# Kernel optimization log

Hardware: AMD Instinct MI355X
Metric: run time of the kernel (lower is better)

## Reference

```python
import jax, jax.numpy as jnp
import numpy as np

IOU_THRESHOLD = 0.5
NEG_POS_RATIO = 3
CENTER_VARIANCE = 0.1
SIZE_VARIANCE = 0.2


def _corner_to_center(b):
    return jnp.concatenate([(b[..., :2] + b[..., 2:]) * 0.5, b[..., 2:] - b[..., :2]], axis=-1)


def _area(lt, rb):
    wh = jnp.clip(rb - lt, 0.0)
    return wh[..., 0] * wh[..., 1]


def _iou(boxes0, boxes1, eps=1e-5):
    lt = jnp.maximum(boxes0[..., :2], boxes1[..., :2])
    rb = jnp.minimum(boxes0[..., 2:], boxes1[..., 2:])
    inter = _area(lt, rb)
    a0 = _area(boxes0[..., :2], boxes0[..., 2:])
    a1 = _area(boxes1[..., :2], boxes1[..., 2:])
    return inter / (a0 + a1 - inter + eps)


def _match_one(gt_boxes, gt_labels, valid, anchors_corner, anchors_center):
    # gt_boxes [G,4] corner, gt_labels [G], valid [G] bool, anchors [A,4]
    G = gt_boxes.shape[0]
    A = anchors_corner.shape[0]
    ious = _iou(gt_boxes[:, None, :], anchors_corner[None, :, :])  # [G, A]
    ious = jnp.where(valid[:, None], ious, -1.0)  # mask padded gts
    best_target_iou = ious.max(axis=0)            # [A]
    best_target_idx = ious.argmax(axis=0)         # [A]
    best_prior_idx = ious.argmax(axis=1)          # [G]
    # force-assign each valid gt to its best anchor (invalid rows -> OOB, dropped)
    safe_prior = jnp.where(valid, best_prior_idx, A)
    best_target_idx = best_target_idx.at[safe_prior].set(jnp.arange(G), mode='drop')
    best_target_iou = best_target_iou.at[safe_prior].set(2.0, mode='drop')
    labels = jnp.where(best_target_iou < IOU_THRESHOLD, 0, gt_labels[best_target_idx])
    boxes_c = _corner_to_center(gt_boxes[best_target_idx])  # [A,4] center form
    loc = jnp.concatenate([
        (boxes_c[:, :2] - anchors_center[:, :2]) / anchors_center[:, 2:] / CENTER_VARIANCE,
        jnp.log(jnp.clip(boxes_c[:, 2:] / anchors_center[:, 2:], 1e-8)) / SIZE_VARIANCE,
    ], axis=-1)
    return labels, loc


def _multibox_loss(confidence, predicted_locations, gts, counts, anchors):
    B, A, C = confidence.shape
    G = gts.shape[1]
    gt_boxes = gts[..., :4]
    gt_labels = gts[..., 4].astype(jnp.int32)
    valid = jnp.arange(G)[None, :] < counts[:, None]  # [B, G]
    anchors_center = _corner_to_center(anchors)
    labels, gt_locations = jax.vmap(_match_one, in_axes=(0, 0, 0, None, None))(
        gt_boxes, gt_labels, valid, anchors, anchors_center)  # [B,A], [B,A,4]

    log_probs = jax.nn.log_softmax(confidence, axis=2)  # [B, A, C]
    bg_loss = -log_probs[:, :, 0]                       # [B, A]
    pos_mask = labels > 0
    num_pos_row = pos_mask.sum(axis=1, keepdims=True)   # [B, 1]
    # hard negative mining: rank background losses per row, keep top 3*num_pos
    mining = jnp.where(pos_mask, -jnp.inf, bg_loss)
    order = jnp.argsort(-mining, axis=1)
    rank = jnp.argsort(order, axis=1)
    neg_mask = rank < num_pos_row * NEG_POS_RATIO
    mask = pos_mask | neg_mask

    num_pos = jnp.maximum(1.0, pos_mask.sum().astype(confidence.dtype))
    ce = -jnp.take_along_axis(log_probs, labels[..., None], axis=2)[..., 0]  # [B, A]
    classification_loss = jnp.where(mask, ce, 0.0).sum() / (num_pos * 4.0)

    diff = jnp.abs(predicted_locations - gt_locations)
    smooth_l1 = jnp.where(diff < 1.0, 0.5 * diff * diff, diff - 0.5)
    localisation_loss = (smooth_l1 * pos_mask[..., None]).sum() / (num_pos * 4.0)
    return localisation_loss, classification_loss


def setup_inputs() -> dict:
    key = jax.random.key(0)
    ks = jax.random.split(key, 8)
    B, A, G, C = 32, 32768, 50, 22
    confidence = jax.random.normal(ks[0], (B, A, C), jnp.float32)
    predicted_locations = jax.random.normal(ks[1], (B, A, 4), jnp.float32)
    a_c = jax.random.uniform(ks[2], (A, 2), minval=0.05, maxval=0.95)
    a_wh = jax.random.uniform(ks[3], (A, 2), minval=0.02, maxval=0.3)
    anchors = jnp.concatenate([jnp.clip(a_c - a_wh * 0.5, 0.0, 1.0),
                               jnp.clip(a_c + a_wh * 0.5, 0.0, 1.0)], axis=-1)
    g_c = jax.random.uniform(ks[4], (B, G, 2), minval=0.1, maxval=0.9)
    g_wh = jax.random.uniform(ks[5], (B, G, 2), minval=0.05, maxval=0.4)
    g_boxes = jnp.concatenate([jnp.clip(g_c - g_wh * 0.5, 0.0, 1.0),
                               jnp.clip(g_c + g_wh * 0.5, 0.0, 1.0)], axis=-1)
    g_labels = jax.random.randint(ks[6], (B, G), 1, C).astype(jnp.float32)
    gts = jnp.concatenate([g_boxes, g_labels[..., None]], axis=-1)
    counts = jax.random.randint(ks[7], (B,), 1, G + 1).astype(jnp.int32)
    return {"confidence": confidence, "predicted_locations": predicted_locations,
            "gts": gts, "counts": counts, "anchors": anchors}


def reference(confidence, predicted_locations, gts, counts, anchors):
    return _multibox_loss(confidence, predicted_locations, gts, counts, anchors)
```

## Files before the change

kernel.cpp:

```cpp
#include <hip/hip_runtime.h>
#include <cstdint>
#include <cstddef>

#define B_N 32
#define A_N 32768
#define G_N 50
#define C_N 22
#define BA  (B_N * A_N)

#define GC 4
#define NCHUNK ((G_N + GC - 1) / GC)
#define ASEG 16
#define ASEG_LEN (A_N / ASEG)

#define SEL_CAP 4096


__device__ __forceinline__ float iou_one(float gx0, float gy0, float gx1, float gy1, float ga,
                                         float ax0, float ay0, float ax1, float ay1, float aa) {
    float lx = fmaxf(gx0, ax0), ly = fmaxf(gy0, ay0);
    float rx = fminf(gx1, ax1), ry = fminf(gy1, ay1);
    float iw = fmaxf(rx - lx, 0.0f), ih = fmaxf(ry - ly, 0.0f);
    float inter = iw * ih;
    return inter / (ga + aa - inter + 1e-5f);
}

__device__ __forceinline__ unsigned int f2key(float x) {
    unsigned int u = __float_as_uint(x);
    return (u & 0x80000000u) ? ~u : (u | 0x80000000u);
}

__device__ __forceinline__ float key2f(unsigned int k) {
    return __uint_as_float((k & 0x80000000u) ? (k & 0x7FFFFFFFu) : ~k);
}


__global__ void init_kernel(float* hdr, unsigned long long* bp_best) {
    if (threadIdx.x < 128) hdr[threadIdx.x] = 0.0f;
    for (int i = threadIdx.x; i < B_N * G_N; i += 256) bp_best[i] = 0ull;
}

__global__ __launch_bounds__(256) void best_prior_kernel(
        const float* __restrict__ gts, const int* __restrict__ counts,
        const float* __restrict__ anchors, unsigned long long* __restrict__ bp_best) {
    int blk = blockIdx.x;
    int b   = blk / (NCHUNK * ASEG);
    int rem = blk % (NCHUNK * ASEG);
    int ch  = rem / ASEG;
    int seg = rem % ASEG;
    int g0  = ch * GC;
    int cnt = counts[b];
    if (g0 >= cnt) return;
    float gx0[GC], gy0[GC], gx1[GC], gy1[GC], ga[GC];
    #pragma unroll
    for (int j = 0; j < GC; ++j) {
        if (g0 + j < cnt) {
            const float* p = gts + (size_t)(b * G_N + g0 + j) * 5;
            gx0[j] = p[0]; gy0[j] = p[1]; gx1[j] = p[2]; gy1[j] = p[3];
            ga[j] = fmaxf(gx1[j] - gx0[j], 0.0f) * fmaxf(gy1[j] - gy0[j], 0.0f);
        } else { gx0[j] = 0.f; gy0[j] = 0.f; gx1[j] = 0.f; gy1[j] = 0.f; ga[j] = 0.f; }
    }
    unsigned long long best[GC];
    #pragma unroll
    for (int j = 0; j < GC; ++j) best[j] = 0ull;
    int a0 = seg * ASEG_LEN;
    for (int a = a0 + threadIdx.x; a < a0 + ASEG_LEN; a += 256) {
        float4 an = reinterpret_cast<const float4*>(anchors)[a];
        float aa = fmaxf(an.z - an.x, 0.0f) * fmaxf(an.w - an.y, 0.0f);
        #pragma unroll
        for (int j = 0; j < GC; ++j) {
            float iou = iou_one(gx0[j], gy0[j], gx1[j], gy1[j], ga[j],
                                an.x, an.y, an.z, an.w, aa);
            unsigned long long key = ((unsigned long long)f2key(iou) << 32) | (unsigned)(~a);
            if (key > best[j]) best[j] = key;
        }
    }
    #pragma unroll
    for (int j = 0; j < GC; ++j) {
        for (int o = 32; o > 0; o >>= 1) {
            unsigned long long other = __shfl_down(best[j], o, 64);
            if (other > best[j]) best[j] = other;
        }
    }
    if ((threadIdx.x & 63) == 0) {
        int ng = cnt - g0; if (ng > GC) ng = GC;
        for (int j = 0; j < ng; ++j)
            atomicMax(&bp_best[b * G_N + g0 + j], best[j]);
    }
}

__global__ __launch_bounds__(256) void fused_kernel(
        const float* __restrict__ gts, const int* __restrict__ counts,
        const float* __restrict__ anchors, const float* __restrict__ pred_loc,
        const float* __restrict__ conf, const unsigned long long* __restrict__ bp_best,
        float* __restrict__ mining, float* __restrict__ loc_part,
        float* __restrict__ ce_part, int* __restrict__ num_pos_row) {
    int blk = blockIdx.x;
    int tid = threadIdx.x;
    int i = blk * 256 + tid;
    int b = blk >> 7;
    int a = i & (A_N - 1);
    int cnt = counts[b];
    __shared__ float sc[256 * C_N];
    __shared__ float sg[G_N][5];
    __shared__ int   sl[G_N];
    __shared__ int   sp[G_N];

    {
        const float4* c4 = reinterpret_cast<const float4*>(conf) + (size_t)blk * (256 * C_N / 4);
        float4* s4 = reinterpret_cast<float4*>(sc);
        #pragma unroll
        for (int t = 0; t < 5; ++t) s4[tid + t * 256] = c4[tid + t * 256];
        if (tid < 128) s4[tid + 5 * 256] = c4[tid + 5 * 256];
    }
    if (tid < G_N) {
        int g = tid;
        const float* gtb = gts + (size_t)(b * G_N + g) * 5;
        float x0 = gtb[0], y0 = gtb[1], x1 = gtb[2], y1 = gtb[3];
        sg[g][0] = x0; sg[g][1] = y0; sg[g][2] = x1; sg[g][3] = y1;
        sg[g][4] = fmaxf(x1 - x0, 0.0f) * fmaxf(y1 - y0, 0.0f);
        sl[g] = (int)gtb[4];
        sp[g] = (int)(~(unsigned)(bp_best[b * G_N + g] & 0xFFFFFFFFull));
    }
    __syncthreads();

    float4 an = reinterpret_cast<const float4*>(anchors)[a];
    float aa = fmaxf(an.z - an.x, 0.0f) * fmaxf(an.w - an.y, 0.0f);
    float best = -2.0f; int gi = 0;
    for (int g = 0; g < cnt; ++g) {
        float iou = iou_one(sg[g][0], sg[g][1], sg[g][2], sg[g][3], sg[g][4],
                            an.x, an.y, an.z, an.w, aa);
        if (iou > best) { best = iou; gi = g; }
    }
    bool forced = false;
    for (int g = 0; g < cnt; ++g) {
        if (sp[g] == a) { gi = g; forced = true; }
    }
    float iou_eff = forced ? 2.0f : best;
    int label = 0;
    if (!(iou_eff < 0.5f)) label = sl[gi];
    bool pos = label > 0;

    float contrib = 0.0f;
    if (pos) {
        float acx = (an.x + an.z) * 0.5f, acy = (an.y + an.w) * 0.5f;
        float aw = an.z - an.x, ah = an.w - an.y;
        float gx0 = sg[gi][0], gy0 = sg[gi][1], gx1 = sg[gi][2], gy1 = sg[gi][3];
        float cx = (gx0 + gx1) * 0.5f, cy = (gy0 + gy1) * 0.5f;
        float w = gx1 - gx0, h = gy1 - gy0;
        float l0 = ((cx - acx) / aw) / 0.1f;
        float l1 = ((cy - acy) / ah) / 0.1f;
        float l2 = logf(fmaxf(w / aw, 1e-8f)) / 0.2f;
        float l3 = logf(fmaxf(h / ah, 1e-8f)) / 0.2f;
        float4 p = reinterpret_cast<const float4*>(pred_loc)[i];
        float d0 = fabsf(p.x - l0), d1 = fabsf(p.y - l1);
        float d2 = fabsf(p.z - l2), d3 = fabsf(p.w - l3);
        contrib  = (d0 < 1.0f ? 0.5f * d0 * d0 : d0 - 0.5f);
        contrib += (d1 < 1.0f ? 0.5f * d1 * d1 : d1 - 0.5f);
        contrib += (d2 < 1.0f ? 0.5f * d2 * d2 : d2 - 0.5f);
        contrib += (d3 < 1.0f ? 0.5f * d3 * d3 : d3 - 0.5f);
    }

    float v[C_N];
    {
        const float2* myrow = reinterpret_cast<const float2*>(sc + tid * C_N);
        #pragma unroll
        for (int j = 0; j < C_N / 2; ++j) { float2 t = myrow[j]; v[2 * j] = t.x; v[2 * j + 1] = t.y; }
    }
    float m = v[0];
    #pragma unroll
    for (int j = 1; j < C_N; ++j) m = fmaxf(m, v[j]);
    float s = 0.0f;
    #pragma unroll
    for (int j = 0; j < C_N; ++j) s += expf(v[j] - m);
    float ls = logf(s);
    float ce_pos = 0.0f;
    if (pos) {
        float vl = v[0];
        #pragma unroll
        for (int j = 1; j < C_N; ++j) vl = (j == label) ? v[j] : vl;
        ce_pos = ls - (vl - m);
        mining[i] = __int_as_float(0xFF800000);
    } else {
        mining[i] = ls - (v[0] - m);
    }

    unsigned long long bal = __ballot(pos);
    for (int o = 32; o > 0; o >>= 1) {
        contrib += __shfl_down(contrib, o, 64);
        ce_pos  += __shfl_down(ce_pos, o, 64);
    }
    __shared__ float swl[4], swc[4];
    __shared__ int   swi[4];
    int wid = tid >> 6, lane = tid & 63;
    if (lane == 0) { swl[wid] = contrib; swc[wid] = ce_pos; swi[wid] = __popcll(bal); }
    __syncthreads();
    if (tid == 0) {
        float sL = swl[0] + swl[1] + swl[2] + swl[3];
        float sC = swc[0] + swc[1] + swc[2] + swc[3];
        int   c  = swi[0] + swi[1] + swi[2] + swi[3];
        int slot = blk & 31;
        if (sL != 0.0f) atomicAdd(&loc_part[slot], sL);
        if (sC != 0.0f) atomicAdd(&ce_part[slot], sC);
        if (c) atomicAdd(&num_pos_row[b], c);
    }
}

__device__ __forceinline__ void scan_pick(unsigned* hist, int nwords,
                                          unsigned* sA, unsigned* sB,
                                          int krem, int* s_bin, int* s_krem) {
    int t = threadIdx.x;
    unsigned lo = 0, hi = 0;
    if (t < nwords) { unsigned w = hist[t]; lo = w & 0xFFFFu; hi = w >> 16; }
    sA[t] = lo + hi;
    __syncthreads();
    unsigned* src = sA; unsigned* dst = sB;
    for (int d = 1; d < 1024; d <<= 1) {
        unsigned vv = src[t] + ((t + d < 1024) ? src[t + d] : 0u);
        dst[t] = vv;
        __syncthreads();
        unsigned* tmp = src; src = dst; dst = tmp;
    }
    unsigned incl = src[t];
    unsigned incl_next = (t < 1023) ? src[t + 1] : 0u;
    unsigned uk = (unsigned)krem;
    if (incl >= uk && incl_next < uk) {
        unsigned cum = incl_next;
        if (cum + hi >= uk) { *s_bin = 2 * t + 1; *s_krem = (int)(uk - cum); }
        else                { *s_bin = 2 * t;     *s_krem = (int)(uk - cum - hi); }
    }
    __syncthreads();
}

__global__ __launch_bounds__(1024) void select_kernel(
        const float* __restrict__ mining, const int* __restrict__ num_pos_row,
        float* __restrict__ neg_sum) {
    int b = blockIdx.x;
    int tid = threadIdx.x;
    int np = num_pos_row[b];
    long long k = 3LL * np;
    int num_neg = A_N - np;
    int k_eff = (int)((k < (long long)num_neg) ? k : (long long)num_neg);
    if (k_eff <= 0) { if (tid == 0) neg_sum[b] = 0.0f; return; }
    const float4* row4 = reinterpret_cast<const float4*>(mining + (size_t)b * A_N);

    __shared__ unsigned hist[1024];
    __shared__ unsigned sA[1024], sB[1024];
    __shared__ unsigned surv[SEL_CAP];
    __shared__ int s_n1, s_bin, s_krem;
    __shared__ float swf[16];

    hist[tid] = 0;
    if (tid == 0) s_n1 = 0;
    __syncthreads();
    #pragma unroll
    for (int it = 0; it < A_N / 4 / 1024; ++it) {
        float4 vv = row4[tid + it * 1024];
        unsigned k0 = f2key(vv.x), k1 = f2key(vv.y), k2 = f2key(vv.z), k3 = f2key(vv.w);
        unsigned b0 = k0 >> 21, b1 = k1 >> 21, b2 = k2 >> 21, b3 = k3 >> 21;
        atomicAdd(&hist[b0 >> 1], (b0 & 1) ? 65536u : 1u);
        atomicAdd(&hist[b1 >> 1], (b1 & 1) ? 65536u : 1u);
        atomicAdd(&hist[b2 >> 1], (b2 & 1) ? 65536u : 1u);
        atomicAdd(&hist[b3 >> 1], (b3 & 1) ? 65536u : 1u);
    }
    __syncthreads();
    scan_pick(hist, 1024, sA, sB, k_eff, &s_bin, &s_krem);
    unsigned bin1 = (unsigned)s_bin;
    int krem1 = s_krem;
    __syncthreads();

    float sum_sel = 0.0f;
    #pragma unroll
    for (int it = 0; it < A_N / 4 / 1024; ++it) {
        float4 vv = row4[tid + it * 1024];
        float xs[4] = {vv.x, vv.y, vv.z, vv.w};
        #pragma unroll
        for (int e = 0; e < 4; ++e) {
            unsigned key = f2key(xs[e]);
            unsigned t11 = key >> 21;
            if (t11 > bin1) sum_sel += xs[e];
            else if (t11 == bin1) {
                int p = atomicAdd(&s_n1, 1);
                if (p < SEL_CAP) surv[p] = key;
            }
        }
    }
    __syncthreads();
    int n1 = s_n1;
    bool in_lds = (n1 <= SEL_CAP);

    hist[tid] = 0;
    __syncthreads();
    if (in_lds) {
        for (int ii = tid; ii < n1; ii += 1024) {
            unsigned bin = (surv[ii] >> 10) & 0x7FFu;
            atomicAdd(&hist[bin >> 1], (bin & 1) ? 65536u : 1u);
        }
    } else {
        for (int it = 0; it < A_N / 4 / 1024; ++it) {
            float4 vv = row4[tid + it * 1024];
            float xs[4] = {vv.x, vv.y, vv.z, vv.w};
            for (int e = 0; e < 4; ++e) {
                unsigned key = f2key(xs[e]);
                if ((key >> 21) == bin1) {
                    unsigned bin = (key >> 10) & 0x7FFu;
                    atomicAdd(&hist[bin >> 1], (bin & 1) ? 65536u : 1u);
                }
            }
        }
    }
    __syncthreads();
    scan_pick(hist, 1024, sA, sB, krem1, &s_bin, &s_krem);
    unsigned prefix22 = (bin1 << 11) | (unsigned)s_bin;
    int krem2 = s_krem;
    __syncthreads();

    hist[tid] = 0;
    __syncthreads();
    if (in_lds) {
        for (int ii = tid; ii < n1; ii += 1024) {
            unsigned key = surv[ii];
            if ((key >> 10) == prefix22) {
                unsigned bin = key & 0x3FFu;
                atomicAdd(&hist[bin >> 1], (bin & 1) ? 65536u : 1u);
            }
        }
    } else {
        for (int it = 0; it < A_N / 4 / 1024; ++it) {
            float4 vv = row4[tid + it * 1024];
            float xs[4] = {vv.x, vv.y, vv.z, vv.w};
            for (int e = 0; e < 4; ++e) {
                unsigned key = f2key(xs[e]);
                if ((key >> 10) == prefix22) {
                    unsigned bin = key & 0x3FFu;
                    atomicAdd(&hist[bin >> 1], (bin & 1) ? 65536u : 1u);
                }
            }
        }
    }
    __syncthreads();
    scan_pick(hist, 512, sA, sB, krem2, &s_bin, &s_krem);
    unsigned kth = (prefix22 << 10) | (unsigned)s_bin;
    int krem3 = s_krem;
    __syncthreads();

    if (in_lds) {
        for (int ii = tid; ii < n1; ii += 1024) {
            unsigned key = surv[ii];
            if (key > kth) sum_sel += key2f(key);
        }
    } else {
        for (int it = 0; it < A_N / 4 / 1024; ++it) {
            float4 vv = row4[tid + it * 1024];
            float xs[4] = {vv.x, vv.y, vv.z, vv.w};
            for (int e = 0; e < 4; ++e) {
                unsigned key = f2key(xs[e]);
                if ((key >> 21) == bin1 && key > kth) sum_sel += xs[e];
            }
        }
    }
    for (int o = 32; o > 0; o >>= 1) sum_sel += __shfl_down(sum_sel, o, 64);
    int wid = tid >> 6, lane = tid & 63;
    if (lane == 0) swf[wid] = sum_sel;
    __syncthreads();
    if (tid == 0) {
        float tot = 0.0f;
        #pragma unroll
        for (int w = 0; w < 16; ++w) tot += swf[w];
        neg_sum[b] = tot + (float)krem3 * key2f(kth);
    }
}

__global__ void final_kernel(const float* __restrict__ loc_part, const float* __restrict__ ce_part,
                             const int* __restrict__ num_pos_row, const float* __restrict__ neg_sum,
                             float* __restrict__ out) {
    if (threadIdx.x != 0) return;
    int tot = 0;
    for (int b = 0; b < B_N; ++b) tot += num_pos_row[b];
    float npos = fmaxf(1.0f, (float)tot);
    float L = 0.0f, Cp = 0.0f, Ng = 0.0f;
    for (int j = 0; j < B_N; ++j) { L += loc_part[j]; Cp += ce_part[j]; Ng += neg_sum[j]; }
    out[0] = L / (npos * 4.0f);
    out[1] = (Cp + Ng) / (npos * 4.0f);
}


extern "C" void kernel_launch(void* const* d_in, const int* in_sizes, int n_in,
                              void* d_out, int out_size, void* d_ws, size_t ws_size,
                              hipStream_t stream) {
    const float* conf     = (const float*)d_in[0];
    const float* pred_loc = (const float*)d_in[1];
    const float* gts      = (const float*)d_in[2];
    const int*   counts   = (const int*)d_in[3];
    const float* anchors  = (const float*)d_in[4];
    float* out = (float*)d_out;

    char* ws = (char*)d_ws;
    float* loc_part     = (float*)ws;
    float* ce_part      = (float*)(ws + 128);
    int*   num_pos_row  = (int*)(ws + 256);
    float* neg_sum      = (float*)(ws + 384);
    unsigned long long* bp_best = (unsigned long long*)(ws + 512);
    float* mining       = (float*)(ws + 16384);

    init_kernel<<<1, 256, 0, stream>>>(loc_part, bp_best);
    best_prior_kernel<<<B_N * NCHUNK * ASEG, 256, 0, stream>>>(gts, counts, anchors, bp_best);
    fused_kernel<<<BA / 256, 256, 0, stream>>>(gts, counts, anchors, pred_loc, conf, bp_best,
                                               mining, loc_part, ce_part, num_pos_row);
    select_kernel<<<B_N, 1024, 0, stream>>>(mining, num_pos_row, neg_sum);
    final_kernel<<<1, 64, 0, stream>>>(loc_part, ce_part, num_pos_row, neg_sum, out);
}
```

Baseline: 263.1 us.

## Process two anchors per thread, drop LDS conf staging, split fused launch

Each thread of the fused kernel now handles two anchors, so each shared gt box read serves two IoU evaluations. The shared-memory staging of confidence rows is removed and rows are read directly from global memory, which frees about 22 KB of LDS per block and may raise occupancy. The fused kernel is issued as four launches of 512 blocks using a block offset. The risks are uncoalesced strided conf loads, higher register pressure, and extra launch overhead.

```diff
diff --git a/kernel.cpp b/kernel.cpp
--- a/kernel.cpp
+++ b/kernel.cpp
@@ -89,30 +89,69 @@
     }
 }
 
+__device__ __forceinline__ void softmax_one(const float* __restrict__ conf, size_t i,
+                                            int lab, bool pos,
+                                            float* __restrict__ mining, float& ce_acc) {
+    float v[C_N];
+    const float2* c2 = reinterpret_cast<const float2*>(conf + i * C_N);
+    #pragma unroll
+    for (int j = 0; j < C_N / 2; ++j) { float2 t = c2[j]; v[2 * j] = t.x; v[2 * j + 1] = t.y; }
+    float m = v[0];
+    #pragma unroll
+    for (int j = 1; j < C_N; ++j) m = fmaxf(m, v[j]);
+    float s = 0.0f;
+    #pragma unroll
+    for (int j = 0; j < C_N; ++j) s += expf(v[j] - m);
+    float ls = logf(s);
+    if (pos) {
+        float vl = v[0];
+        #pragma unroll
+        for (int j = 1; j < C_N; ++j) vl = (j == lab) ? v[j] : vl;
+        ce_acc += ls - (vl - m);
+        mining[i] = __int_as_float(0xFF800000);
+    } else {
+        mining[i] = ls - (v[0] - m);
+    }
+}
+
+__device__ __forceinline__ float loc_term(float4 an, const float sgrow[5],
+                                          const float* __restrict__ pred_loc, size_t i) {
+    float acx = (an.x + an.z) * 0.5f, acy = (an.y + an.w) * 0.5f;
+    float aw = an.z - an.x, ah = an.w - an.y;
+    float gx0 = sgrow[0], gy0 = sgrow[1], gx1 = sgrow[2], gy1 = sgrow[3];
+    float cx = (gx0 + gx1) * 0.5f, cy = (gy0 + gy1) * 0.5f;
+    float w = gx1 - gx0, h = gy1 - gy0;
+    float l0 = ((cx - acx) / aw) / 0.1f;
+    float l1 = ((cy - acy) / ah) / 0.1f;
+    float l2 = logf(fmaxf(w / aw, 1e-8f)) / 0.2f;
+    float l3 = logf(fmaxf(h / ah, 1e-8f)) / 0.2f;
+    float4 p = reinterpret_cast<const float4*>(pred_loc)[i];
+    float d0 = fabsf(p.x - l0), d1 = fabsf(p.y - l1);
+    float d2 = fabsf(p.z - l2), d3 = fabsf(p.w - l3);
+    float c;
+    c  = (d0 < 1.0f ? 0.5f * d0 * d0 : d0 - 0.5f);
+    c += (d1 < 1.0f ? 0.5f * d1 * d1 : d1 - 0.5f);
+    c += (d2 < 1.0f ? 0.5f * d2 * d2 : d2 - 0.5f);
+    c += (d3 < 1.0f ? 0.5f * d3 * d3 : d3 - 0.5f);
+    return c;
+}
+
 __global__ __launch_bounds__(256) void fused_kernel(
         const float* __restrict__ gts, const int* __restrict__ counts,
         const float* __restrict__ anchors, const float* __restrict__ pred_loc,
         const float* __restrict__ conf, const unsigned long long* __restrict__ bp_best,
         float* __restrict__ mining, float* __restrict__ loc_part,
-        float* __restrict__ ce_part, int* __restrict__ num_pos_row) {
-    int blk = blockIdx.x;
+        float* __restrict__ ce_part, int* __restrict__ num_pos_row, int blk_off) {
+    int blk = blockIdx.x + blk_off;
     int tid = threadIdx.x;
-    int i = blk * 256 + tid;
-    int b = blk >> 7;
-    int a = i & (A_N - 1);
+    int b = blk >> 6;
+    int abase = (blk & 63) << 9;
+    int a0 = abase + tid, a1 = a0 + 256;
+    size_t i0 = (size_t)b * A_N + a0, i1 = i0 + 256;
     int cnt = counts[b];
-    __shared__ float sc[256 * C_N];
     __shared__ float sg[G_N][5];
     __shared__ int   sl[G_N];
     __shared__ int   sp[G_N];
-
-    {
-        const float4* c4 = reinterpret_cast<const float4*>(conf) + (size_t)blk * (256 * C_N / 4);
-        float4* s4 = reinterpret_cast<float4*>(sc);
-        #pragma unroll
-        for (int t = 0; t < 5; ++t) s4[tid + t * 256] = c4[tid + t * 256];
-        if (tid < 128) s4[tid + 5 * 256] = c4[tid + 5 * 256];
-    }
     if (tid < G_N) {
         int g = tid;
         const float* gtb = gts + (size_t)(b * G_N + g) * 5;
@@ -124,76 +163,49 @@
     }
     __syncthreads();
 
-    float4 an = reinterpret_cast<const float4*>(anchors)[a];
-    float aa = fmaxf(an.z - an.x, 0.0f) * fmaxf(an.w - an.y, 0.0f);
-    float best = -2.0f; int gi = 0;
+    float4 an0 = reinterpret_cast<const float4*>(anchors)[a0];
+    float4 an1 = reinterpret_cast<const float4*>(anchors)[a1];
+    float aa0 = fmaxf(an0.z - an0.x, 0.0f) * fmaxf(an0.w - an0.y, 0.0f);
+    float aa1 = fmaxf(an1.z - an1.x, 0.0f) * fmaxf(an1.w - an1.y, 0.0f);
+    float best0 = -2.0f, best1 = -2.0f;
+    int gi0 = 0, gi1 = 0;
     for (int g = 0; g < cnt; ++g) {
-        float iou = iou_one(sg[g][0], sg[g][1], sg[g][2], sg[g][3], sg[g][4],
-                            an.x, an.y, an.z, an.w, aa);
-        if (iou > best) { best = iou; gi = g; }
-    }
-    bool forced = false;
+        float x0 = sg[g][0], y0 = sg[g][1], x1 = sg[g][2], y1 = sg[g][3], ar = sg[g][4];
+        float iou0 = iou_one(x0, y0, x1, y1, ar, an0.x, an0.y, an0.z, an0.w, aa0);
+        float iou1 = iou_one(x0, y0, x1, y1, ar, an1.x, an1.y, an1.z, an1.w, aa1);
+        if (iou0 > best0) { best0 = iou0; gi0 = g; }
+        if (iou1 > best1) { best1 = iou1; gi1 = g; }
+    }
+    bool f0 = false, f1 = false;
     for (int g = 0; g < cnt; ++g) {
-        if (sp[g] == a) { gi = g; forced = true; }
-    }
-    float iou_eff = forced ? 2.0f : best;
-    int label = 0;
-    if (!(iou_eff < 0.5f)) label = sl[gi];
-    bool pos = label > 0;
+        int p = sp[g];
+        if (p == a0) { gi0 = g; f0 = true; }
+        if (p == a1) { gi1 = g; f1 = true; }
+    }
+    float ie0 = f0 ? 2.0f : best0;
+    float ie1 = f1 ? 2.0f : best1;
+    int lab0 = 0; if (!(ie0 < 0.5f)) lab0 = sl[gi0];
+    int lab1 = 0; if (!(ie1 < 0.5f)) lab1 = sl[gi1];
+    bool pos0 = lab0 > 0, pos1 = lab1 > 0;
 
     float contrib = 0.0f;
-    if (pos) {
-        float acx = (an.x + an.z) * 0.5f, acy = (an.y + an.w) * 0.5f;
-        float aw = an.z - an.x, ah = an.w - an.y;
-        float gx0 = sg[gi][0], gy0 = sg[gi][1], gx1 = sg[gi][2], gy1 = sg[gi][3];
-        float cx = (gx0 + gx1) * 0.5f, cy = (gy0 + gy1) * 0.5f;
-        float w = gx1 - gx0, h = gy1 - gy0;
-        float l0 = ((cx - acx) / aw) / 0.1f;
-        float l1 = ((cy - acy) / ah) / 0.1f;
-        float l2 = logf(fmaxf(w / aw, 1e-8f)) / 0.2f;
-        float l3 = logf(fmaxf(h / ah, 1e-8f)) / 0.2f;
-        float4 p = reinterpret_cast<const float4*>(pred_loc)[i];
-        float d0 = fabsf(p.x - l0), d1 = fabsf(p.y - l1);
-        float d2 = fabsf(p.z - l2), d3 = fabsf(p.w - l3);
-        contrib  = (d0 < 1.0f ? 0.5f * d0 * d0 : d0 - 0.5f);
-        contrib += (d1 < 1.0f ? 0.5f * d1 * d1 : d1 - 0.5f);
-        contrib += (d2 < 1.0f ? 0.5f * d2 * d2 : d2 - 0.5f);
-        contrib += (d3 < 1.0f ? 0.5f * d3 * d3 : d3 - 0.5f);
-    }
-
-    float v[C_N];
-    {
-        const float2* myrow = reinterpret_cast<const float2*>(sc + tid * C_N);
-        #pragma unroll
-        for (int j = 0; j < C_N / 2; ++j) { float2 t = myrow[j]; v[2 * j] = t.x; v[2 * j + 1] = t.y; }
-    }
-    float m = v[0];
-    #pragma unroll
-    for (int j = 1; j < C_N; ++j) m = fmaxf(m, v[j]);
-    float s = 0.0f;
-    #pragma unroll
-    for (int j = 0; j < C_N; ++j) s += expf(v[j] - m);
-    float ls = logf(s);
-    float ce_pos = 0.0f;
-    if (pos) {
-        float vl = v[0];
-        #pragma unroll
-        for (int j = 1; j < C_N; ++j) vl = (j == label) ? v[j] : vl;
-        ce_pos = ls - (vl - m);
-        mining[i] = __int_as_float(0xFF800000);
-    } else {
-        mining[i] = ls - (v[0] - m);
-    }
-
-    unsigned long long bal = __ballot(pos);
+    if (pos0) contrib += loc_term(an0, sg[gi0], pred_loc, i0);
+    if (pos1) contrib += loc_term(an1, sg[gi1], pred_loc, i1);
+
+    float ce = 0.0f;
+    softmax_one(conf, i0, lab0, pos0, mining, ce);
+    softmax_one(conf, i1, lab1, pos1, mining, ce);
+
+    unsigned long long bal0 = __ballot(pos0);
+    unsigned long long bal1 = __ballot(pos1);
     for (int o = 32; o > 0; o >>= 1) {
         contrib += __shfl_down(contrib, o, 64);
-        ce_pos  += __shfl_down(ce_pos, o, 64);
+        ce      += __shfl_down(ce, o, 64);
     }
     __shared__ float swl[4], swc[4];
     __shared__ int   swi[4];
     int wid = tid >> 6, lane = tid & 63;
-    if (lane == 0) { swl[wid] = contrib; swc[wid] = ce_pos; swi[wid] = __popcll(bal); }
+    if (lane == 0) { swl[wid] = contrib; swc[wid] = ce; swi[wid] = __popcll(bal0) + __popcll(bal1); }
     __syncthreads();
     if (tid == 0) {
         float sL = swl[0] + swl[1] + swl[2] + swl[3];
@@ -405,8 +417,10 @@
 
     init_kernel<<<1, 256, 0, stream>>>(loc_part, bp_best);
     best_prior_kernel<<<B_N * NCHUNK * ASEG, 256, 0, stream>>>(gts, counts, anchors, bp_best);
-    fused_kernel<<<BA / 256, 256, 0, stream>>>(gts, counts, anchors, pred_loc, conf, bp_best,
-                                               mining, loc_part, ce_part, num_pos_row);
+    for (int p = 0; p < 4; ++p) {
+        fused_kernel<<<512, 256, 0, stream>>>(gts, counts, anchors, pred_loc, conf, bp_best,
+                                              mining, loc_part, ce_part, num_pos_row, p * 512);
+    }
     select_kernel<<<B_N, 1024, 0, stream>>>(mining, num_pos_row, neg_sum);
     final_kernel<<<1, 64, 0, stream>>>(loc_part, ce_part, num_pos_row, neg_sum, out);
 }
```

New measurement: 261.5 us. About the same (-0.6%).
